# Kernel tuning notes

Hardware: AMD Instinct MI355X
Metric: run time of the kernel (lower is better)

The kernel has to match this reference:

```python
import jax, jax.numpy as jnp
import numpy as np

B, N_OBS = 4096, 64
H = 256
SCALE = 0.05  # keep activations stable through SQUARE/MUL layers


def setup_inputs() -> dict:
    key = jax.random.key(0)
    ks = jax.random.split(key, 16)
    rn = lambda k, shp, s=SCALE: s * jax.random.normal(k, shp, dtype=jnp.float32)
    return {
        "x": jax.random.normal(ks[0], (B, N_OBS), dtype=jnp.float32),
        "xdot": jax.random.normal(ks[1], (B, N_OBS), dtype=jnp.float32),
        "w1": rn(ks[2], (H, N_OBS)), "b1": rn(ks[3], (H,)),
        "w2a": rn(ks[4], (H, H)), "b2a": rn(ks[5], (H,)),
        "w2b": rn(ks[6], (H, H)), "b2b": rn(ks[7], (H,)),
        "w3a": rn(ks[8], (H, H)), "b3a": rn(ks[9], (H,)),
        "w3s": rn(ks[10], (H, N_OBS)), "b3s": rn(ks[11], (H,)),
        "wout": rn(ks[12], (1, H)),
        "scalar": jax.random.normal(ks[13], (1,), dtype=jnp.float32),
    }


def reference(x, xdot, w1, b1, w2a, b2a, w2b, b2b, w3a, b3a, w3s, b3s, wout, scalar):
    # mul path: empty mul_activation -> yy = x*0 + scalar  (shape [B, n_obs])
    yy = x * 0 + scalar

    # Layer 1: SQUARE. Initial jac is identity, so
    # matmul(2*diag(z), W1) @ I == 2*z[:,:,None] * W1
    z = x @ w1.T + b1                      # [B, H]
    y = z * z
    jac = (2.0 * z)[:, :, None] * w1[None]  # [B, H, N_OBS]

    # Layer 2: MUL. diag(z1)@W2b + diag(z2)@W2a == z1[:,:,None]*w2b + z2[:,:,None]*w2a
    z1 = y @ w2a.T + b2a
    z2 = y @ w2b.T + b2b
    y = z1 * z2
    grad = z1[:, :, None] * w2b[None] + z2[:, :, None] * w2a[None]  # [B, H, H]
    jac = jnp.einsum('boh,bhi->boi', grad, jac)                      # [B, H, N_OBS]

    # Layer 3: SKIP. jac = diag(z1)@W3s + (diag(z2)@W3a)@jac
    z1 = y @ w3a.T + b3a
    z2 = x @ w3s.T + b3s
    y = z1 * z2
    jac = z1[:, :, None] * w3s[None] + z2[:, :, None] * jnp.einsum('oh,bhi->boi', w3a, jac)

    numerical_b = y @ wout.T                                # [B, 1]
    jac = jnp.einsum('oh,bhi->boi', wout, jac)              # [B, 1, N_OBS]
    numerical_bdot = jnp.sum(jac[:, 0, :] * xdot, axis=1)   # [B]
    return (numerical_b, numerical_bdot, y, yy)
```

## Files before the change

kernel.cpp:

```cpp
#include <hip/hip_runtime.h>

typedef unsigned short ushort_t;
typedef unsigned int uint_t;
typedef __bf16 bf16x8 __attribute__((ext_vector_type(8)));
typedef float f32x4 __attribute__((ext_vector_type(4)));

#define H 256
#define RPB 16
#define NBLK 256

#define NB_OFF 0
#define BDOT_OFF 4096
#define Y_OFF 8192
#define YY_OFF (8192 + 4096 * 256)

__device__ __forceinline__ ushort_t f2bf(float x) {
    union { float f; uint_t u; } c; c.f = x;
    uint_t r = (c.u + 0x7FFFu + ((c.u >> 16) & 1u)) >> 16;
    return (ushort_t)r;
}
__device__ __forceinline__ float bf2f(ushort_t v) {
    union { uint_t u; float f; } c; c.u = ((uint_t)v) << 16;
    return c.f;
}

#define O_W1b  0
#define O_W1T  16384
#define O_W2ab 32768
#define O_W2bb 98304
#define O_W3ab 163840
#define O_W2aT 229376
#define O_W2bT 294912
#define O_W3aT 360448
#define O_W3sb 425984
#define O_W3sT 442368

__global__ __launch_bounds__(256) void prep_weights(
    const float* __restrict__ w1, const float* __restrict__ w2a,
    const float* __restrict__ w2b, const float* __restrict__ w3a,
    const float* __restrict__ w3s, const float* __restrict__ wout,
    ushort_t* __restrict__ ws) {
    __shared__ float tile[32][65];
    int b = blockIdx.x;
    const float* src; int Oo, Ot, C, t; bool scl;
    if (b < 32)       { src = w2a; Oo = O_W2ab; Ot = O_W2aT; C = 256; t = b;       scl = false; }
    else if (b < 64)  { src = w2b; Oo = O_W2bb; Ot = O_W2bT; C = 256; t = b - 32;  scl = false; }
    else if (b < 96)  { src = w3a; Oo = O_W3ab; Ot = O_W3aT; C = 256; t = b - 64;  scl = true;  }
    else if (b < 104) { src = w1;  Oo = O_W1b;  Ot = O_W1T;  C = 64;  t = b - 96;  scl = false; }
    else              { src = w3s; Oo = O_W3sb; Ot = O_W3sT; C = 64;  t = b - 104; scl = true;  }
    int tr, tc;
    if (C == 256) { tr = t >> 2; tc = t & 3; } else { tr = t; tc = 0; }
    int r0 = tr * 32, c0 = tc * 64;
    const int tid = threadIdx.x;

    union pack8 { ushort_t u[8]; uint4 q; };
    {
        int r = tid >> 3, c8 = (tid & 7) << 3;
        const float* s = src + (r0 + r) * C + c0 + c8;
        pack8 p;
#pragma unroll
        for (int j = 0; j < 8; j++) { float v = s[j]; tile[r][c8 + j] = v; p.u[j] = f2bf(v); }
        *(uint4*)(ws + Oo + (r0 + r) * C + c0 + c8) = p.q;
    }
    __syncthreads();
    {
        int cc = tid >> 2, r8 = (tid & 3) << 3;
        pack8 p;
#pragma unroll
        for (int j = 0; j < 8; j++) {
            float v = tile[r8 + j][cc];
            if (scl) v *= wout[r0 + r8 + j];
            p.u[j] = f2bf(v);
        }
        *(uint4*)(ws + Ot + (c0 + cc) * 256 + r0 + r8) = p.q;
    }
}

#define RS 5
#define RA 4
#define U_RING 0
#define U_Z    40960
#define U_Y    45056
#define U_Z12  49152
#define U_Z22  53248
#define U_Z23  57344
#define U_U    61440
#define U_XD   65536
#define U_NB   69632
#define SMEM_USHORTS 69664
#define SMEM_BYTES (SMEM_USHORTS * 2)

__device__ __forceinline__ void gload16(const ushort_t* g, ushort_t* l) {
    __builtin_amdgcn_global_load_lds(
        (const __attribute__((address_space(1))) void*)g,
        (__attribute__((address_space(3))) void*)l, 16, 0, 0);
}

template <int N> __device__ __forceinline__ void vwait() {
    if constexpr (N == 3) asm volatile("s_waitcnt vmcnt(3)" ::: "memory");
    else if constexpr (N == 2) asm volatile("s_waitcnt vmcnt(2)" ::: "memory");
    else if constexpr (N == 1) asm volatile("s_waitcnt vmcnt(1)" ::: "memory");
    else asm volatile("s_waitcnt vmcnt(0)" ::: "memory");
}

#define PHASE_BARRIER() do { \
    asm volatile("s_waitcnt lgkmcnt(0)" ::: "memory"); \
    __builtin_amdgcn_sched_barrier(0); \
    __builtin_amdgcn_s_barrier(); \
    __builtin_amdgcn_sched_barrier(0); \
} while (0)

__device__ __forceinline__ int posw(int r, int c) { return r * H + (c ^ ((r & 7) << 3)); }

template <int P, bool SUM>
__device__ __forceinline__ void ring_phase(
    const ushort_t* __restrict__ gm0, const ushort_t* __restrict__ gm1,
    const ushort_t* __restrict__ gn0, const ushort_t* __restrict__ gn1,
    const ushort_t* aP0, const ushort_t* aP1,
    ushort_t* rw, int srcoff, int boff, int kq, int sw,
    f32x4& acc0, f32x4& acc1) {
#pragma unroll
    for (int k = 0; k < 16; ++k) {
        const int u = P * 16 + k;
        if (P == 2) {
            if (k < 13) vwait<3>();
            else if (k == 13) vwait<2>();
            else if (k == 14) vwait<1>();
            else vwait<0>();
        } else {
            vwait<3>();
        }
        __builtin_amdgcn_sched_barrier(0);
        bf16x8 b = *(const bf16x8*)(rw + (u % RS) * 512 + boff);
        const ushort_t* ap = (k & 1) ? aP1 : aP0;
        bf16x8 a = *(const bf16x8*)(ap + ((((k >> 1) << 5) + kq) ^ sw));
        if (u + RA < 48) {
            asm volatile("s_waitcnt lgkmcnt(2)" ::: "memory");
            __builtin_amdgcn_sched_barrier(0);
            const int k4 = k + RA;
            const ushort_t* g = (k4 < 16) ? ((k4 & 1) ? gm1 : gm0)
                                          : ((k4 & 1) ? gn1 : gn0);
            const int cc = (k4 & 15) >> 1;
            gload16(g + srcoff + (cc << 5), rw + ((u + RA) % RS) * 512);
        }
        if (SUM)
            acc0 = __builtin_amdgcn_mfma_f32_16x16x32_bf16(a, b, acc0, 0, 0, 0);
        else if ((k & 1) == 0)
            acc0 = __builtin_amdgcn_mfma_f32_16x16x32_bf16(a, b, acc0, 0, 0, 0);
        else
            acc1 = __builtin_amdgcn_mfma_f32_16x16x32_bf16(a, b, acc1, 0, 0, 0);
    }
}

template <int NF, int STRA, int STRB>
__device__ __forceinline__ void gemm_one(const ushort_t* sA, const ushort_t* __restrict__ B0,
                                         int lane, int k0, f32x4& acc0) {
    const int row = lane & 15;
    const int kq = (lane >> 4) << 3;
    const int sw = (row & 7) << 3;
    bf16x8 b0[NF], a[NF];
    const ushort_t* bp0 = B0 + row * STRB + k0 + kq;
    const ushort_t* ap = sA + row * STRA;
#pragma unroll
    for (int i = 0; i < NF; i++) b0[i] = *(const bf16x8*)(bp0 + i * 32);
#pragma unroll
    for (int i = 0; i < NF; i++) a[i] = *(const bf16x8*)(ap + ((k0 + i * 32 + kq) ^ sw));
    __builtin_amdgcn_sched_barrier(0);
#pragma unroll
    for (int i = 0; i < NF; i++)
        acc0 = __builtin_amdgcn_mfma_f32_16x16x32_bf16(a[i], b0[i], acc0, 0, 0, 0);
}

__global__ __launch_bounds__(1024) void net_main(
    const float* __restrict__ x, const float* __restrict__ xd,
    const float* __restrict__ b1, const float* __restrict__ b2a,
    const float* __restrict__ b2b, const float* __restrict__ b3a,
    const float* __restrict__ b3s, const float* __restrict__ wout,
    const float* __restrict__ scalar, const ushort_t* __restrict__ ws,
    float* __restrict__ out) {
    extern __shared__ __align__(16) ushort_t smem[];
    ushort_t* sZ   = smem + U_Z;
    ushort_t* sY   = smem + U_Y;
    ushort_t* sZ12 = smem + U_Z12;
    ushort_t* sZ22 = smem + U_Z22;
    ushort_t* sZ23 = smem + U_Z23;
    ushort_t* sU   = smem + U_U;
    float* sXd = (float*)(smem + U_XD);
    float* sNB = (float*)(smem + U_NB);

    const int tid = threadIdx.x;
    const int wid = tid >> 6;
    const int lane = tid & 63;
    const int row16 = lane & 15;
    const int rq = lane >> 4;
    const int R0 = blockIdx.x * RPB;
    const int n0 = wid * 16;
    const int kq = rq << 3;
    const int sw = (row16 & 7) << 3;

    ushort_t* rw = smem + U_RING + wid * (RS * 512);
    const int srcoff = ((wid << 4) + (lane >> 2)) * 256 + (lane & 3) * 8;
    const int boff = row16 * 32 + rq * 8;

    const ushort_t* gW2ab = ws + O_W2ab;
    const ushort_t* gW2bb = ws + O_W2bb;
    const ushort_t* gW3ab = ws + O_W3ab;
    const ushort_t* gW3aT = ws + O_W3aT;
    const ushort_t* gW2bT = ws + O_W2bT;
    const ushort_t* gW2aT = ws + O_W2aT;

    f32x4 y3keep;
    {
        const ushort_t* w1p = ws + O_W1b + (n0 + row16) * 64 + kq;
        const ushort_t* w3p = ws + O_W3sb + (n0 + row16) * 64 + kq;
        bf16x8 pb0 = *(const bf16x8*)(w1p);
        bf16x8 pb1 = *(const bf16x8*)(w1p + 32);
        bf16x8 pb2 = *(const bf16x8*)(w3p);
        bf16x8 pb3 = *(const bf16x8*)(w3p + 32);
        const float* xg = x + (R0 + row16) * 64;
        float4 x0 = *(const float4*)(xg + kq);
        float4 x1 = *(const float4*)(xg + kq + 4);
        float4 x2 = *(const float4*)(xg + 32 + kq);
        float4 x3 = *(const float4*)(xg + 32 + kq + 4);
        int xr = tid >> 6, xc = tid & 63;
        float xdv = xd[(R0 + xr) * 64 + xc];
        float sc = scalar[0];
        gload16(gW2ab + srcoff, rw);
        gload16(gW2bb + srcoff, rw + 512);
        gload16(gW2ab + srcoff + 32, rw + 1024);
        gload16(gW2bb + srcoff + 32, rw + 1536);
        __builtin_amdgcn_sched_barrier(0);
        out[YY_OFF + (R0 + xr) * 64 + xc] = sc;
        sXd[tid] = xdv;
        if (tid < RPB) sNB[tid] = 0.f;
        union { ushort_t u[8]; bf16x8 v; } A0, A1;
#pragma unroll
        for (int j = 0; j < 4; j++) {
            A0.u[j]     = f2bf(((const float*)&x0)[j]);
            A0.u[4 + j] = f2bf(((const float*)&x1)[j]);
            A1.u[j]     = f2bf(((const float*)&x2)[j]);
            A1.u[4 + j] = f2bf(((const float*)&x3)[j]);
        }
        f32x4 z = {0.f,0.f,0.f,0.f}, q = {0.f,0.f,0.f,0.f};
        z = __builtin_amdgcn_mfma_f32_16x16x32_bf16(A0.v, pb0, z, 0, 0, 0);
        z = __builtin_amdgcn_mfma_f32_16x16x32_bf16(A1.v, pb1, z, 0, 0, 0);
        q = __builtin_amdgcn_mfma_f32_16x16x32_bf16(A0.v, pb2, q, 0, 0, 0);
        q = __builtin_amdgcn_mfma_f32_16x16x32_bf16(A1.v, pb3, q, 0, 0, 0);
        int c = n0 + row16;
        float bz = b1[c], bs = b3s[c];
#pragma unroll
        for (int i = 0; i < 4; i++) {
            int r = rq * 4 + i;
            int p = posw(r, c);
            float za = z[i] + bz;
            sZ[p] = f2bf(za);
            sY[p] = f2bf(za * za);
            sZ23[p] = f2bf(q[i] + bs);
        }
    }
    PHASE_BARRIER();

    const ushort_t* aRow = (const ushort_t*)0;
    (void)aRow;
    const int arow = row16 * H;

    {
        f32x4 aA = {0.f,0.f,0.f,0.f}, aB = {0.f,0.f,0.f,0.f};
        ring_phase<0, false>(gW2ab, gW2bb, gW3ab, gW3aT, sY + arow, sY + arow,
                             rw, srcoff, boff, kq, sw, aA, aB);
        int c = n0 + row16;
        float ba = b2a[c], bb = b2b[c];
#pragma unroll
        for (int i = 0; i < 4; i++) {
            int r = rq * 4 + i;
            int p = posw(r, c);
            float z12 = aA[i] + ba, z22 = aB[i] + bb;
            sZ12[p] = f2bf(z12);
            sZ22[p] = f2bf(z22);
            sU[p] = f2bf(z12 * z22);
        }
    }
    PHASE_BARRIER();

    {
        f32x4 zz = {0.f,0.f,0.f,0.f}, tt = {0.f,0.f,0.f,0.f};
        ring_phase<1, false>(gW3ab, gW3aT, gW2bT, gW2aT, sU + arow, sZ23 + arow,
                             rw, srcoff, boff, kq, sw, zz, tt);
        int c = n0 + row16;
        float ba = b3a[c], wo = wout[c];
#pragma unroll
        for (int i = 0; i < 4; i++) {
            int r = rq * 4 + i;
            int p = posw(r, c);
            float z13 = zz[i] + ba;
            float z23 = bf2f(sZ23[p]);
            float y3 = z13 * z23;
            y3keep[i] = y3;
            sY[p] = f2bf(z13);
            float t = tt[i];
            sZ12[p] = f2bf(t * bf2f(sZ12[p]));
            sZ22[p] = f2bf(t * bf2f(sZ22[p]));
            float v = wo * y3;
            v += __shfl_xor(v, 1);
            v += __shfl_xor(v, 2);
            v += __shfl_xor(v, 4);
            v += __shfl_xor(v, 8);
            if (row16 == 0) atomicAdd(&sNB[r], v);
        }
    }
    PHASE_BARRIER();

    {
        f32x4 pp = {0.f,0.f,0.f,0.f}, dummy = {0.f,0.f,0.f,0.f};
        ring_phase<2, true>(gW2bT, gW2aT, gW2bT, gW2aT, sZ12 + arow, sZ22 + arow,
                            rw, srcoff, boff, kq, sw, pp, dummy);
        int c = n0 + row16;
#pragma unroll
        for (int i = 0; i < 4; i++) {
            int r = rq * 4 + i;
            int p = posw(r, c);
            sZ[p] = f2bf(2.f * pp[i] * bf2f(sZ[p]));
        }
    }
    PHASE_BARRIER();

    {
        int c = n0 + row16;
#pragma unroll
        for (int i = 0; i < 4; i++)
            out[Y_OFF + (R0 + rq * 4 + i) * H + c] = y3keep[i];
        int mat = wid >> 3, kh = (wid >> 2) & 1, nt = wid & 3;
        const ushort_t* A = mat ? sZ : sY;
        const ushort_t* B = ws + (mat ? O_W1T : O_W3sT) + nt * 16 * H;
        f32x4 acc = {0.f,0.f,0.f,0.f};
        gemm_one<4, H, H>(A, B, lane, kh * 128, acc);
        float* F01 = (float*)sZ23;
        float* F23 = (float*)sU;
        float* dst = mat ? (F23 + kh * 1024) : (F01 + kh * 1024);
        int cc = nt * 16 + row16;
#pragma unroll
        for (int i = 0; i < 4; i++) dst[(rq * 4 + i) * 64 + cc] = acc[i];
    }
    PHASE_BARRIER();

    {
        float* F0 = (float*)sZ23;
        float* F1 = F0 + 1024;
        float* F2 = (float*)sU;
        float* F3 = F2 + 1024;
        int r = tid >> 6, j = tid & 63;
        int e = r * 64 + j;
        float s = (F0[e] + F1[e] + F2[e] + F3[e]) * sXd[e];
        s += __shfl_xor(s, 1);
        s += __shfl_xor(s, 2);
        s += __shfl_xor(s, 4);
        s += __shfl_xor(s, 8);
        s += __shfl_xor(s, 16);
        s += __shfl_xor(s, 32);
        if (j == 0) out[BDOT_OFF + R0 + r] = s;
        if (tid < RPB) out[NB_OFF + R0 + tid] = sNB[tid];
    }
}

extern "C" void kernel_launch(void* const* d_in, const int* in_sizes, int n_in,
                              void* d_out, int out_size, void* d_ws, size_t ws_size,
                              hipStream_t stream) {
    (void)in_sizes; (void)n_in; (void)out_size; (void)ws_size;
    const float* x = (const float*)d_in[0];
    const float* xd = (const float*)d_in[1];
    const float* w1 = (const float*)d_in[2];
    const float* b1 = (const float*)d_in[3];
    const float* w2a = (const float*)d_in[4];
    const float* b2a = (const float*)d_in[5];
    const float* w2b = (const float*)d_in[6];
    const float* b2b = (const float*)d_in[7];
    const float* w3a = (const float*)d_in[8];
    const float* b3a = (const float*)d_in[9];
    const float* w3s = (const float*)d_in[10];
    const float* b3s = (const float*)d_in[11];
    const float* wout = (const float*)d_in[12];
    const float* scalar = (const float*)d_in[13];
    ushort_t* ws = (ushort_t*)d_ws;
    float* out = (float*)d_out;

    static bool attr_set = false;
    if (!attr_set) {
        hipFuncSetAttribute((const void*)net_main,
                            hipFuncAttributeMaxDynamicSharedMemorySize, SMEM_BYTES);
        attr_set = true;
    }

    prep_weights<<<112, 256, 0, stream>>>(w1, w2a, w2b, w3a, w3s, wout, ws);
    net_main<<<NBLK, 1024, SMEM_BYTES, stream>>>(x, xd, b1, b2a, b2b, b3a, b3s, wout, scalar, ws, out);
}
```

Measured before the change: 31.21 us.

## Process 32 rows per block so each streamed weight tile feeds two MFMAs

Doubles rows per block from 16 to 32 and halves the grid to 128 blocks. Each weight B-fragment streamed through the LDS ring now feeds two MFMAs (two row groups), halving global weight traffic per row. The ring shrinks from 5 to 4 slots with power-of-two indexing and an XOR swizzle on the ring layout to cut LDS bank conflicts. The z1 buffer is kept in registers instead of LDS. The risk is lower parallelism on a GPU with more CUs than the new block count, plus higher register and LDS pressure.

Result: slower. 35.33 us (+13.2%).

```diff
diff --git a/kernel.cpp b/kernel.cpp
--- a/kernel.cpp
+++ b/kernel.cpp
@@ -6,8 +6,8 @@
 typedef float f32x4 __attribute__((ext_vector_type(4)));
 
 #define H 256
-#define RPB 16
-#define NBLK 256
+#define RPB 32
+#define NBLK 128
 
 #define NB_OFF 0
 #define BDOT_OFF 4096
@@ -76,18 +76,17 @@
     }
 }
 
-#define RS 5
+#define RS 4
 #define RA 4
 #define U_RING 0
-#define U_Z    40960
-#define U_Y    45056
-#define U_Z12  49152
-#define U_Z22  53248
+#define U_Y    32768
+#define U_Z12  40960
+#define U_Z22  49152
 #define U_Z23  57344
-#define U_U    61440
-#define U_XD   65536
-#define U_NB   69632
-#define SMEM_USHORTS 69664
+#define U_U    65536
+#define U_XD   73728
+#define U_NB   77824
+#define SMEM_USHORTS 77888
 #define SMEM_BYTES (SMEM_USHORTS * 2)
 
 __device__ __forceinline__ void gload16(const ushort_t* g, ushort_t* l) {
@@ -116,9 +115,11 @@
 __device__ __forceinline__ void ring_phase(
     const ushort_t* __restrict__ gm0, const ushort_t* __restrict__ gm1,
     const ushort_t* __restrict__ gn0, const ushort_t* __restrict__ gn1,
-    const ushort_t* aP0, const ushort_t* aP1,
+    const ushort_t* aM0, const ushort_t* aM1,
     ushort_t* rw, int srcoff, int boff, int kq, int sw,
-    f32x4& acc0, f32x4& acc1) {
+    f32x4& a00, f32x4& a01, f32x4& a10, f32x4& a11) {
+    const int arow0 = ( boff >> 5) * H;
+    const int arow1 = arow0 + 16 * H;
 #pragma unroll
     for (int k = 0; k < 16; ++k) {
         const int u = P * 16 + k;
@@ -131,9 +132,11 @@
             vwait<3>();
         }
         __builtin_amdgcn_sched_barrier(0);
-        bf16x8 b = *(const bf16x8*)(rw + (u % RS) * 512 + boff);
-        const ushort_t* ap = (k & 1) ? aP1 : aP0;
-        bf16x8 a = *(const bf16x8*)(ap + ((((k >> 1) << 5) + kq) ^ sw));
+        bf16x8 b = *(const bf16x8*)(rw + (u & 3) * 512 + boff);
+        const ushort_t* am = (k & 1) ? aM1 : aM0;
+        const int ko = (((k >> 1) << 5) + kq) ^ sw;
+        bf16x8 a0 = *(const bf16x8*)(am + arow0 + ko);
+        bf16x8 a1 = *(const bf16x8*)(am + arow1 + ko);
         if (u + RA < 48) {
             asm volatile("s_waitcnt lgkmcnt(2)" ::: "memory");
             __builtin_amdgcn_sched_barrier(0);
@@ -141,14 +144,15 @@
             const ushort_t* g = (k4 < 16) ? ((k4 & 1) ? gm1 : gm0)
                                           : ((k4 & 1) ? gn1 : gn0);
             const int cc = (k4 & 15) >> 1;
-            gload16(g + srcoff + (cc << 5), rw + ((u + RA) % RS) * 512);
-        }
-        if (SUM)
-            acc0 = __builtin_amdgcn_mfma_f32_16x16x32_bf16(a, b, acc0, 0, 0, 0);
-        else if ((k & 1) == 0)
-            acc0 = __builtin_amdgcn_mfma_f32_16x16x32_bf16(a, b, acc0, 0, 0, 0);
-        else
-            acc1 = __builtin_amdgcn_mfma_f32_16x16x32_bf16(a, b, acc1, 0, 0, 0);
+            gload16(g + srcoff + (cc << 5), rw + ((u + RA) & 3) * 512);
+        }
+        if ((k & 1) == 0 || SUM) {
+            a00 = __builtin_amdgcn_mfma_f32_16x16x32_bf16(a0, b, a00, 0, 0, 0);
+            a01 = __builtin_amdgcn_mfma_f32_16x16x32_bf16(a1, b, a01, 0, 0, 0);
+        } else {
+            a10 = __builtin_amdgcn_mfma_f32_16x16x32_bf16(a0, b, a10, 0, 0, 0);
+            a11 = __builtin_amdgcn_mfma_f32_16x16x32_bf16(a1, b, a11, 0, 0, 0);
+        }
     }
 }
 
@@ -179,7 +183,6 @@
     const float* __restrict__ scalar, const ushort_t* __restrict__ ws,
     float* __restrict__ out) {
     extern __shared__ __align__(16) ushort_t smem[];
-    ushort_t* sZ   = smem + U_Z;
     ushort_t* sY   = smem + U_Y;
     ushort_t* sZ12 = smem + U_Z12;
     ushort_t* sZ22 = smem + U_Z22;
@@ -199,8 +202,9 @@
     const int sw = (row16 & 7) << 3;
 
     ushort_t* rw = smem + U_RING + wid * (RS * 512);
-    const int srcoff = ((wid << 4) + (lane >> 2)) * 256 + (lane & 3) * 8;
-    const int boff = row16 * 32 + rq * 8;
+    const int nsrc = (wid << 4) + (lane >> 2);
+    const int srcoff = nsrc * 256 + (((lane & 3) ^ (nsrc & 3)) << 3);
+    const int boff = row16 * 32 + (kq ^ ((row16 & 3) << 3));
 
     const ushort_t* gW2ab = ws + O_W2ab;
     const ushort_t* gW2bb = ws + O_W2bb;
@@ -209,117 +213,139 @@
     const ushort_t* gW2bT = ws + O_W2bT;
     const ushort_t* gW2aT = ws + O_W2aT;
 
-    f32x4 y3keep;
-    {
+    f32x4 zk0, zk1, y3k0, y3k1;
+
+    {
+        float sc = scalar[0];
+        int xr = tid >> 6, xc = tid & 63;
+        float xd0 = xd[(R0 + xr) * 64 + xc];
+        float xd1 = xd[(R0 + 16 + xr) * 64 + xc];
+        out[YY_OFF + (R0 + xr) * 64 + xc] = sc;
+        out[YY_OFF + (R0 + 16 + xr) * 64 + xc] = sc;
         const ushort_t* w1p = ws + O_W1b + (n0 + row16) * 64 + kq;
         const ushort_t* w3p = ws + O_W3sb + (n0 + row16) * 64 + kq;
         bf16x8 pb0 = *(const bf16x8*)(w1p);
         bf16x8 pb1 = *(const bf16x8*)(w1p + 32);
         bf16x8 pb2 = *(const bf16x8*)(w3p);
         bf16x8 pb3 = *(const bf16x8*)(w3p + 32);
-        const float* xg = x + (R0 + row16) * 64;
-        float4 x0 = *(const float4*)(xg + kq);
-        float4 x1 = *(const float4*)(xg + kq + 4);
-        float4 x2 = *(const float4*)(xg + 32 + kq);
-        float4 x3 = *(const float4*)(xg + 32 + kq + 4);
-        int xr = tid >> 6, xc = tid & 63;
-        float xdv = xd[(R0 + xr) * 64 + xc];
-        float sc = scalar[0];
+        const float* xg0 = x + (R0 + row16) * 64;
+        const float* xg1 = x + (R0 + 16 + row16) * 64;
+        float4 xa0 = *(const float4*)(xg0 + kq);
+        float4 xa1 = *(const float4*)(xg0 + kq + 4);
+        float4 xa2 = *(const float4*)(xg0 + 32 + kq);
+        float4 xa3 = *(const float4*)(xg0 + 32 + kq + 4);
+        float4 xb0 = *(const float4*)(xg1 + kq);
+        float4 xb1 = *(const float4*)(xg1 + kq + 4);
+        float4 xb2 = *(const float4*)(xg1 + 32 + kq);
+        float4 xb3 = *(const float4*)(xg1 + 32 + kq + 4);
+        __builtin_amdgcn_sched_barrier(0);
         gload16(gW2ab + srcoff, rw);
         gload16(gW2bb + srcoff, rw + 512);
         gload16(gW2ab + srcoff + 32, rw + 1024);
         gload16(gW2bb + srcoff + 32, rw + 1536);
         __builtin_amdgcn_sched_barrier(0);
-        out[YY_OFF + (R0 + xr) * 64 + xc] = sc;
-        sXd[tid] = xdv;
+        sXd[tid] = xd0;
+        sXd[tid + 1024] = xd1;
         if (tid < RPB) sNB[tid] = 0.f;
-        union { ushort_t u[8]; bf16x8 v; } A0, A1;
+        union { ushort_t u[8]; bf16x8 v; } A0, A1, B0v, B1v;
 #pragma unroll
         for (int j = 0; j < 4; j++) {
-            A0.u[j]     = f2bf(((const float*)&x0)[j]);
-            A0.u[4 + j] = f2bf(((const float*)&x1)[j]);
-            A1.u[j]     = f2bf(((const float*)&x2)[j]);
-            A1.u[4 + j] = f2bf(((const float*)&x3)[j]);
-        }
-        f32x4 z = {0.f,0.f,0.f,0.f}, q = {0.f,0.f,0.f,0.f};
-        z = __builtin_amdgcn_mfma_f32_16x16x32_bf16(A0.v, pb0, z, 0, 0, 0);
-        z = __builtin_amdgcn_mfma_f32_16x16x32_bf16(A1.v, pb1, z, 0, 0, 0);
-        q = __builtin_amdgcn_mfma_f32_16x16x32_bf16(A0.v, pb2, q, 0, 0, 0);
-        q = __builtin_amdgcn_mfma_f32_16x16x32_bf16(A1.v, pb3, q, 0, 0, 0);
+            A0.u[j]      = f2bf(((const float*)&xa0)[j]);
+            A0.u[4 + j]  = f2bf(((const float*)&xa1)[j]);
+            A1.u[j]      = f2bf(((const float*)&xa2)[j]);
+            A1.u[4 + j]  = f2bf(((const float*)&xa3)[j]);
+            B0v.u[j]     = f2bf(((const float*)&xb0)[j]);
+            B0v.u[4 + j] = f2bf(((const float*)&xb1)[j]);
+            B1v.u[j]     = f2bf(((const float*)&xb2)[j]);
+            B1v.u[4 + j] = f2bf(((const float*)&xb3)[j]);
+        }
+        f32x4 z0 = {0.f,0.f,0.f,0.f}, z1 = {0.f,0.f,0.f,0.f};
+        f32x4 q0 = {0.f,0.f,0.f,0.f}, q1 = {0.f,0.f,0.f,0.f};
+        z0 = __builtin_amdgcn_mfma_f32_16x16x32_bf16(A0.v, pb0, z0, 0, 0, 0);
+        z0 = __builtin_amdgcn_mfma_f32_16x16x32_bf16(A1.v, pb1, z0, 0, 0, 0);
+        z1 = __builtin_amdgcn_mfma_f32_16x16x32_bf16(B0v.v, pb0, z1, 0, 0, 0);
+        z1 = __builtin_amdgcn_mfma_f32_16x16x32_bf16(B1v.v, pb1, z1, 0, 0, 0);
+        q0 = __builtin_amdgcn_mfma_f32_16x16x32_bf16(A0.v, pb2, q0, 0, 0, 0);
+        q0 = __builtin_amdgcn_mfma_f32_16x16x32_bf16(A1.v, pb3, q0, 0, 0, 0);
+        q1 = __builtin_amdgcn_mfma_f32_16x16x32_bf16(B0v.v, pb2, q1, 0, 0, 0);
+        q1 = __builtin_amdgcn_mfma_f32_16x16x32_bf16(B1v.v, pb3, q1, 0, 0, 0);
         int c = n0 + row16;
         float bz = b1[c], bs = b3s[c];
 #pragma unroll
         for (int i = 0; i < 4; i++) {
             int r = rq * 4 + i;
-            int p = posw(r, c);
-            float za = z[i] + bz;
-            sZ[p] = f2bf(za);
-            sY[p] = f2bf(za * za);
-            sZ23[p] = f2bf(q[i] + bs);
+            int p0 = posw(r, c), p1 = posw(r + 16, c);
+            float za = z0[i] + bz, zb = z1[i] + bz;
+            zk0[i] = za; zk1[i] = zb;
+            sY[p0] = f2bf(za * za);
+            sY[p1] = f2bf(zb * zb);
+            sZ23[p0] = f2bf(q0[i] + bs);
+            sZ23[p1] = f2bf(q1[i] + bs);
         }
     }
     PHASE_BARRIER();
 
-    const ushort_t* aRow = (const ushort_t*)0;
-    (void)aRow;
-    const int arow = row16 * H;
-
-    {
-        f32x4 aA = {0.f,0.f,0.f,0.f}, aB = {0.f,0.f,0.f,0.f};
-        ring_phase<0, false>(gW2ab, gW2bb, gW3ab, gW3aT, sY + arow, sY + arow,
-                             rw, srcoff, boff, kq, sw, aA, aB);
+    {
+        f32x4 a00 = {0.f,0.f,0.f,0.f}, a01 = {0.f,0.f,0.f,0.f};
+        f32x4 a10 = {0.f,0.f,0.f,0.f}, a11 = {0.f,0.f,0.f,0.f};
+        ring_phase<0, false>(gW2ab, gW2bb, gW3ab, gW3aT, sY, sY,
+                             rw, srcoff, boff, kq, sw, a00, a01, a10, a11);
         int c = n0 + row16;
         float ba = b2a[c], bb = b2b[c];
 #pragma unroll
         for (int i = 0; i < 4; i++) {
             int r = rq * 4 + i;
-            int p = posw(r, c);
-            float z12 = aA[i] + ba, z22 = aB[i] + bb;
-            sZ12[p] = f2bf(z12);
-            sZ22[p] = f2bf(z22);
-            sU[p] = f2bf(z12 * z22);
+            int p0 = posw(r, c), p1 = posw(r + 16, c);
+            float z12a = a00[i] + ba, z22a = a10[i] + bb;
+            float z12b = a01[i] + ba, z22b = a11[i] + bb;
+            sZ12[p0] = f2bf(z12a); sZ22[p0] = f2bf(z22a); sU[p0] = f2bf(z12a * z22a);
+            sZ12[p1] = f2bf(z12b); sZ22[p1] = f2bf(z22b); sU[p1] = f2bf(z12b * z22b);
         }
     }
     PHASE_BARRIER();
 
     {
-        f32x4 zz = {0.f,0.f,0.f,0.f}, tt = {0.f,0.f,0.f,0.f};
-        ring_phase<1, false>(gW3ab, gW3aT, gW2bT, gW2aT, sU + arow, sZ23 + arow,
-                             rw, srcoff, boff, kq, sw, zz, tt);
+        f32x4 zz0 = {0.f,0.f,0.f,0.f}, zz1 = {0.f,0.f,0.f,0.f};
+        f32x4 tt0 = {0.f,0.f,0.f,0.f}, tt1 = {0.f,0.f,0.f,0.f};
+        ring_phase<1, false>(gW3ab, gW3aT, gW2bT, gW2aT, sU, sZ23,
+                             rw, srcoff, boff, kq, sw, zz0, zz1, tt0, tt1);
         int c = n0 + row16;
         float ba = b3a[c], wo = wout[c];
 #pragma unroll
         for (int i = 0; i < 4; i++) {
             int r = rq * 4 + i;
-            int p = posw(r, c);
-            float z13 = zz[i] + ba;
-            float z23 = bf2f(sZ23[p]);
-            float y3 = z13 * z23;
-            y3keep[i] = y3;
-            sY[p] = f2bf(z13);
-            float t = tt[i];
-            sZ12[p] = f2bf(t * bf2f(sZ12[p]));
-            sZ22[p] = f2bf(t * bf2f(sZ22[p]));
-            float v = wo * y3;
-            v += __shfl_xor(v, 1);
-            v += __shfl_xor(v, 2);
-            v += __shfl_xor(v, 4);
-            v += __shfl_xor(v, 8);
-            if (row16 == 0) atomicAdd(&sNB[r], v);
+            int p0 = posw(r, c), p1 = posw(r + 16, c);
+            float z13a = zz0[i] + ba, z23a = bf2f(sZ23[p0]);
+            float z13b = zz1[i] + ba, z23b = bf2f(sZ23[p1]);
+            float y3a = z13a * z23a, y3b = z13b * z23b;
+            y3k0[i] = y3a; y3k1[i] = y3b;
+            sY[p0] = f2bf(z13a);
+            sY[p1] = f2bf(z13b);
+            sZ12[p0] = f2bf(tt0[i] * bf2f(sZ12[p0]));
+            sZ22[p0] = f2bf(tt0[i] * bf2f(sZ22[p0]));
+            sZ12[p1] = f2bf(tt1[i] * bf2f(sZ12[p1]));
+            sZ22[p1] = f2bf(tt1[i] * bf2f(sZ22[p1]));
+            float v0 = wo * y3a, v1 = wo * y3b;
+            v0 += __shfl_xor(v0, 1); v0 += __shfl_xor(v0, 2);
+            v0 += __shfl_xor(v0, 4); v0 += __shfl_xor(v0, 8);
+            v1 += __shfl_xor(v1, 1); v1 += __shfl_xor(v1, 2);
+            v1 += __shfl_xor(v1, 4); v1 += __shfl_xor(v1, 8);
+            if (row16 == 0) { atomicAdd(&sNB[r], v0); atomicAdd(&sNB[r + 16], v1); }
         }
     }
     PHASE_BARRIER();
 
     {
-        f32x4 pp = {0.f,0.f,0.f,0.f}, dummy = {0.f,0.f,0.f,0.f};
-        ring_phase<2, true>(gW2bT, gW2aT, gW2bT, gW2aT, sZ12 + arow, sZ22 + arow,
-                            rw, srcoff, boff, kq, sw, pp, dummy);
+        f32x4 pp0 = {0.f,0.f,0.f,0.f}, pp1 = {0.f,0.f,0.f,0.f};
+        f32x4 d0 = {0.f,0.f,0.f,0.f}, d1 = {0.f,0.f,0.f,0.f};
+        ring_phase<2, true>(gW2bT, gW2aT, gW2bT, gW2aT, sZ12, sZ22,
+                            rw, srcoff, boff, kq, sw, pp0, pp1, d0, d1);
         int c = n0 + row16;
 #pragma unroll
         for (int i = 0; i < 4; i++) {
             int r = rq * 4 + i;
-            int p = posw(r, c);
-            sZ[p] = f2bf(2.f * pp[i] * bf2f(sZ[p]));
+            sU[posw(r, c)] = f2bf(2.f * pp0[i] * zk0[i]);
+            sU[posw(r + 16, c)] = f2bf(2.f * pp1[i] * zk1[i]);
         }
     }
     PHASE_BARRIER();
@@ -327,36 +353,40 @@
     {
         int c = n0 + row16;
 #pragma unroll
-        for (int i = 0; i < 4; i++)
-            out[Y_OFF + (R0 + rq * 4 + i) * H + c] = y3keep[i];
+        for (int i = 0; i < 4; i++) {
+            out[Y_OFF + (R0 + rq * 4 + i) * H + c] = y3k0[i];
+            out[Y_OFF + (R0 + 16 + rq * 4 + i) * H + c] = y3k1[i];
+        }
         int mat = wid >> 3, kh = (wid >> 2) & 1, nt = wid & 3;
-        const ushort_t* A = mat ? sZ : sY;
+        const ushort_t* Abase = mat ? sU : sY;
         const ushort_t* B = ws + (mat ? O_W1T : O_W3sT) + nt * 16 * H;
-        f32x4 acc = {0.f,0.f,0.f,0.f};
-        gemm_one<4, H, H>(A, B, lane, kh * 128, acc);
-        float* F01 = (float*)sZ23;
-        float* F23 = (float*)sU;
-        float* dst = mat ? (F23 + kh * 1024) : (F01 + kh * 1024);
+        float* dst = (float*)(mat ? sZ22 : sZ12) + kh * 2048;
         int cc = nt * 16 + row16;
 #pragma unroll
-        for (int i = 0; i < 4; i++) dst[(rq * 4 + i) * 64 + cc] = acc[i];
+        for (int rg = 0; rg < 2; rg++) {
+            f32x4 acc = {0.f,0.f,0.f,0.f};
+            gemm_one<4, H, H>(Abase + rg * 16 * H, B, lane, kh * 128, acc);
+#pragma unroll
+            for (int i = 0; i < 4; i++)
+                dst[(rg * 16 + rq * 4 + i) * 64 + cc] = acc[i];
+        }
     }
     PHASE_BARRIER();
 
     {
-        float* F0 = (float*)sZ23;
-        float* F1 = F0 + 1024;
-        float* F2 = (float*)sU;
-        float* F3 = F2 + 1024;
-        int r = tid >> 6, j = tid & 63;
-        int e = r * 64 + j;
-        float s = (F0[e] + F1[e] + F2[e] + F3[e]) * sXd[e];
+        float* F0 = (float*)sZ12;
+        float* F1 = F0 + 2048;
+        float* F2 = (float*)sZ22;
+        float* F3 = F2 + 2048;
+        int r = tid >> 5, j = tid & 31;
+        int e = r * 64 + j, e2 = e + 32;
+        float s = (F0[e] + F1[e] + F2[e] + F3[e]) * sXd[e] +
+                  (F0[e2] + F1[e2] + F2[e2] + F3[e2]) * sXd[e2];
         s += __shfl_xor(s, 1);
         s += __shfl_xor(s, 2);
         s += __shfl_xor(s, 4);
         s += __shfl_xor(s, 8);
         s += __shfl_xor(s, 16);
-        s += __shfl_xor(s, 32);
         if (j == 0) out[BDOT_OFF + R0 + r] = s;
         if (tid < RPB) out[NB_OFF + R0 + tid] = sNB[tid];
     }
```

## Split weight streaming between LDS ring and direct-to-register loads per phase

Applied to the files above, without the earlier changes.

Replaces the 5-slot LDS ring, which staged both weight matrices of each phase, with a hybrid scheme. One matrix still streams through a 4-slot swizzled LDS ring via global_load_lds, while the paired matrix is loaded straight into registers three steps ahead. This halves LDS ring traffic and shrinks shared memory, which could raise occupancy, at the cost of more registers and exposed global-load latency on the register path. The LDS ring layout also gains an XOR swizzle to reduce bank conflicts.

New measurement: 33.40 us. 1.07x slower.

```diff
diff --git a/kernel.cpp b/kernel.cpp
--- a/kernel.cpp
+++ b/kernel.cpp
@@ -76,18 +76,16 @@
     }
 }
 
-#define RS 5
-#define RA 4
 #define U_RING 0
-#define U_Z    40960
-#define U_Y    45056
-#define U_Z12  49152
-#define U_Z22  53248
-#define U_Z23  57344
-#define U_U    61440
-#define U_XD   65536
-#define U_NB   69632
-#define SMEM_USHORTS 69664
+#define U_Z    32768
+#define U_Y    36864
+#define U_Z12  40960
+#define U_Z22  45056
+#define U_Z23  49152
+#define U_U    53248
+#define U_XD   57344
+#define U_NB   59392
+#define SMEM_USHORTS 59424
 #define SMEM_BYTES (SMEM_USHORTS * 2)
 
 __device__ __forceinline__ void gload16(const ushort_t* g, ushort_t* l) {
@@ -97,9 +95,8 @@
 }
 
 template <int N> __device__ __forceinline__ void vwait() {
-    if constexpr (N == 3) asm volatile("s_waitcnt vmcnt(3)" ::: "memory");
+    if constexpr (N == 4) asm volatile("s_waitcnt vmcnt(4)" ::: "memory");
     else if constexpr (N == 2) asm volatile("s_waitcnt vmcnt(2)" ::: "memory");
-    else if constexpr (N == 1) asm volatile("s_waitcnt vmcnt(1)" ::: "memory");
     else asm volatile("s_waitcnt vmcnt(0)" ::: "memory");
 }
 
@@ -112,43 +109,45 @@
 
 __device__ __forceinline__ int posw(int r, int c) { return r * H + (c ^ ((r & 7) << 3)); }
 
-template <int P, bool SUM>
-__device__ __forceinline__ void ring_phase(
-    const ushort_t* __restrict__ gm0, const ushort_t* __restrict__ gm1,
-    const ushort_t* __restrict__ gn0, const ushort_t* __restrict__ gn1,
-    const ushort_t* aP0, const ushort_t* aP1,
-    ushort_t* rw, int srcoff, int boff, int kq, int sw,
-    f32x4& acc0, f32x4& acc1) {
-#pragma unroll
-    for (int k = 0; k < 16; ++k) {
-        const int u = P * 16 + k;
+template <int P, int LG>
+__device__ __forceinline__ void hybrid_phase(
+    const ushort_t* __restrict__ gm, const ushort_t* __restrict__ rm,
+    const ushort_t* __restrict__ gn, const ushort_t* __restrict__ rn,
+    const ushort_t* aD, const ushort_t* aR,
+    ushort_t* rw, int srcoff, int regoff, int boff, int kq, int sw,
+    bf16x8 (&breg)[4], f32x4& accD, f32x4& accR) {
+#pragma unroll
+    for (int k = 0; k < 8; ++k) {
+        const int u = P * 8 + k;
         if (P == 2) {
-            if (k < 13) vwait<3>();
-            else if (k == 13) vwait<2>();
-            else if (k == 14) vwait<1>();
+            if (k <= 5) vwait<4>();
+            else if (k == 6) vwait<2>();
             else vwait<0>();
         } else {
-            vwait<3>();
-        }
-        __builtin_amdgcn_sched_barrier(0);
-        bf16x8 b = *(const bf16x8*)(rw + (u % RS) * 512 + boff);
-        const ushort_t* ap = (k & 1) ? aP1 : aP0;
-        bf16x8 a = *(const bf16x8*)(ap + ((((k >> 1) << 5) + kq) ^ sw));
-        if (u + RA < 48) {
-            asm volatile("s_waitcnt lgkmcnt(2)" ::: "memory");
+            vwait<4>();
+        }
+        __builtin_amdgcn_sched_barrier(0);
+        bf16x8 bD = *(const bf16x8*)(rw + (u & 3) * 512 + boff);
+        const int ko = ((k << 5) + kq) ^ sw;
+        bf16x8 aDv = *(const bf16x8*)(aD + ko);
+        bf16x8 aRv;
+        if constexpr (LG == 3) aRv = *(const bf16x8*)(aR + ko);
+        else aRv = aDv;
+        bf16x8 bR = breg[u & 3];
+        if (u + 3 < 24) {
+            if constexpr (LG == 2) asm volatile("s_waitcnt lgkmcnt(2)" ::: "memory");
+            else                   asm volatile("s_waitcnt lgkmcnt(3)" ::: "memory");
             __builtin_amdgcn_sched_barrier(0);
-            const int k4 = k + RA;
-            const ushort_t* g = (k4 < 16) ? ((k4 & 1) ? gm1 : gm0)
-                                          : ((k4 & 1) ? gn1 : gn0);
-            const int cc = (k4 & 15) >> 1;
-            gload16(g + srcoff + (cc << 5), rw + ((u + RA) % RS) * 512);
-        }
-        if (SUM)
-            acc0 = __builtin_amdgcn_mfma_f32_16x16x32_bf16(a, b, acc0, 0, 0, 0);
-        else if ((k & 1) == 0)
-            acc0 = __builtin_amdgcn_mfma_f32_16x16x32_bf16(a, b, acc0, 0, 0, 0);
-        else
-            acc1 = __builtin_amdgcn_mfma_f32_16x16x32_bf16(a, b, acc1, 0, 0, 0);
+            const int k3 = k + 3;
+            const ushort_t* gsrc = (k3 < 8) ? gm : gn;
+            const ushort_t* rsrc = (k3 < 8) ? rm : rn;
+            const int cc = k3 & 7;
+            gload16(gsrc + srcoff + (cc << 5), rw + ((u + 3) & 3) * 512);
+            breg[(u + 3) & 3] = *(const bf16x8*)(rsrc + regoff + (cc << 5));
+            __builtin_amdgcn_sched_barrier(0);
+        }
+        accD = __builtin_amdgcn_mfma_f32_16x16x32_bf16(aDv, bD, accD, 0, 0, 0);
+        accR = __builtin_amdgcn_mfma_f32_16x16x32_bf16(aRv, bR, accR, 0, 0, 0);
     }
 }
 
@@ -198,9 +197,12 @@
     const int kq = rq << 3;
     const int sw = (row16 & 7) << 3;
 
-    ushort_t* rw = smem + U_RING + wid * (RS * 512);
-    const int srcoff = ((wid << 4) + (lane >> 2)) * 256 + (lane & 3) * 8;
-    const int boff = row16 * 32 + rq * 8;
+    ushort_t* rw = smem + U_RING + wid * 2048;
+    const int nsrc = (wid << 4) + (lane >> 2);
+    const int srcoff = nsrc * 256 + (((lane & 3) ^ (nsrc & 3)) << 3);
+    const int boff = row16 * 32 + (kq ^ ((row16 & 3) << 3));
+    const int regoff = (n0 + row16) * 256 + kq;
+    const int arow = row16 * H;
 
     const ushort_t* gW2ab = ws + O_W2ab;
     const ushort_t* gW2bb = ws + O_W2bb;
@@ -210,6 +212,8 @@
     const ushort_t* gW2aT = ws + O_W2aT;
 
     f32x4 y3keep;
+    bf16x8 breg[4];
+
     {
         const ushort_t* w1p = ws + O_W1b + (n0 + row16) * 64 + kq;
         const ushort_t* w3p = ws + O_W3sb + (n0 + row16) * 64 + kq;
@@ -225,12 +229,20 @@
         int xr = tid >> 6, xc = tid & 63;
         float xdv = xd[(R0 + xr) * 64 + xc];
         float sc = scalar[0];
+        out[YY_OFF + (R0 + xr) * 64 + xc] = sc;
+        __builtin_amdgcn_sched_barrier(0);
         gload16(gW2ab + srcoff, rw);
-        gload16(gW2bb + srcoff, rw + 512);
-        gload16(gW2ab + srcoff + 32, rw + 1024);
-        gload16(gW2bb + srcoff + 32, rw + 1536);
-        __builtin_amdgcn_sched_barrier(0);
-        out[YY_OFF + (R0 + xr) * 64 + xc] = sc;
+        __builtin_amdgcn_sched_barrier(0);
+        breg[0] = *(const bf16x8*)(gW2bb + regoff);
+        __builtin_amdgcn_sched_barrier(0);
+        gload16(gW2ab + srcoff + 32, rw + 512);
+        __builtin_amdgcn_sched_barrier(0);
+        breg[1] = *(const bf16x8*)(gW2bb + regoff + 32);
+        __builtin_amdgcn_sched_barrier(0);
+        gload16(gW2ab + srcoff + 64, rw + 1024);
+        __builtin_amdgcn_sched_barrier(0);
+        breg[2] = *(const bf16x8*)(gW2bb + regoff + 64);
+        __builtin_amdgcn_sched_barrier(0);
         sXd[tid] = xdv;
         if (tid < RPB) sNB[tid] = 0.f;
         union { ushort_t u[8]; bf16x8 v; } A0, A1;
@@ -260,14 +272,10 @@
     }
     PHASE_BARRIER();
 
-    const ushort_t* aRow = (const ushort_t*)0;
-    (void)aRow;
-    const int arow = row16 * H;
-
     {
         f32x4 aA = {0.f,0.f,0.f,0.f}, aB = {0.f,0.f,0.f,0.f};
-        ring_phase<0, false>(gW2ab, gW2bb, gW3ab, gW3aT, sY + arow, sY + arow,
-                             rw, srcoff, boff, kq, sw, aA, aB);
+        hybrid_phase<0, 2>(gW2ab, gW2bb, gW3ab, gW3aT, sY + arow, sY + arow,
+                           rw, srcoff, regoff, boff, kq, sw, breg, aA, aB);
         int c = n0 + row16;
         float ba = b2a[c], bb = b2b[c];
 #pragma unroll
@@ -284,8 +292,8 @@
 
     {
         f32x4 zz = {0.f,0.f,0.f,0.f}, tt = {0.f,0.f,0.f,0.f};
-        ring_phase<1, false>(gW3ab, gW3aT, gW2bT, gW2aT, sU + arow, sZ23 + arow,
-                             rw, srcoff, boff, kq, sw, zz, tt);
+        hybrid_phase<1, 3>(gW3ab, gW3aT, gW2bT, gW2aT, sU + arow, sZ23 + arow,
+                           rw, srcoff, regoff, boff, kq, sw, breg, zz, tt);
         int c = n0 + row16;
         float ba = b3a[c], wo = wout[c];
 #pragma unroll
@@ -311,15 +319,15 @@
     PHASE_BARRIER();
 
     {
-        f32x4 pp = {0.f,0.f,0.f,0.f}, dummy = {0.f,0.f,0.f,0.f};
-        ring_phase<2, true>(gW2bT, gW2aT, gW2bT, gW2aT, sZ12 + arow, sZ22 + arow,
-                            rw, srcoff, boff, kq, sw, pp, dummy);
+        f32x4 pD = {0.f,0.f,0.f,0.f}, pR = {0.f,0.f,0.f,0.f};
+        hybrid_phase<2, 3>(gW2bT, gW2aT, gW2bT, gW2aT, sZ12 + arow, sZ22 + arow,
+                           rw, srcoff, regoff, boff, kq, sw, breg, pD, pR);
         int c = n0 + row16;
 #pragma unroll
         for (int i = 0; i < 4; i++) {
             int r = rq * 4 + i;
             int p = posw(r, c);
-            sZ[p] = f2bf(2.f * pp[i] * bf2f(sZ[p]));
+            sZ[p] = f2bf(2.f * (pD[i] + pR[i]) * bf2f(sZ[p]));
         }
     }
     PHASE_BARRIER();
```

## Pre-tile weights into contiguous swizzled chunks and rotate K order per block

Applied to the files above, without the earlier changes.

The prep kernel now writes the 256x256 weights as per-wave, per-K-chunk contiguous 1KB tiles, with an XOR swizzle on the 8-element groups. The main kernel's ring loads therefore read contiguous global memory, and the matching swizzled LDS offset is meant to cut bank conflicts. Each block also starts its K loop at a chunk rotated by blockIdx, which spreads simultaneous L2 accesses across blocks. This adds a more complex prep kernel with strided transposed reads, and leaves an unused ring_phase variant behind.

After: 29.58 us. 1.06x faster.

```diff
diff --git a/kernel.cpp b/kernel.cpp
--- a/kernel.cpp
+++ b/kernel.cpp
@@ -24,14 +24,14 @@
     return c.f;
 }
 
-#define O_W1b  0
-#define O_W1T  16384
-#define O_W2ab 32768
-#define O_W2bb 98304
-#define O_W3ab 163840
-#define O_W2aT 229376
-#define O_W2bT 294912
-#define O_W3aT 360448
+#define T_W2A  0
+#define T_W2B  65536
+#define T_W3A  131072
+#define T_W2BT 196608
+#define T_W2AT 262144
+#define T_W3AT 327680
+#define O_W1b  393216
+#define O_W1T  409600
 #define O_W3sb 425984
 #define O_W3sT 442368
 
@@ -40,27 +40,44 @@
     const float* __restrict__ w2b, const float* __restrict__ w3a,
     const float* __restrict__ w3s, const float* __restrict__ wout,
     ushort_t* __restrict__ ws) {
+    const int b = blockIdx.x;
+    const int tid = threadIdx.x;
+    if (b < 96) {
+        const int m = b >> 4, t = b & 15;
+        const float* src; int dst; bool isT, scl;
+        switch (m) {
+            case 0: src = w2a; dst = T_W2A;  isT = false; scl = false; break;
+            case 1: src = w2b; dst = T_W2B;  isT = false; scl = false; break;
+            case 2: src = w3a; dst = T_W3A;  isT = false; scl = false; break;
+            case 3: src = w2b; dst = T_W2BT; isT = true;  scl = false; break;
+            case 4: src = w2a; dst = T_W2AT; isT = true;  scl = false; break;
+            default: src = w3a; dst = T_W3AT; isT = true; scl = true;  break;
+        }
+        for (int idx = tid; idx < 4096; idx += 256) {
+            int c = idx >> 9, rem = idx & 511;
+            int l = rem >> 3, j = rem & 7;
+            int r = l >> 2, o = (l & 3) ^ (r & 3);
+            int gk = c * 32 + o * 8 + j;
+            int row = t * 16 + r;
+            float v = isT ? src[gk * 256 + row] : src[row * 256 + gk];
+            if (scl) v *= wout[gk];
+            ws[dst + t * 4096 + idx] = f2bf(v);
+        }
+        return;
+    }
     __shared__ float tile[32][65];
-    int b = blockIdx.x;
-    const float* src; int Oo, Ot, C, t; bool scl;
-    if (b < 32)       { src = w2a; Oo = O_W2ab; Ot = O_W2aT; C = 256; t = b;       scl = false; }
-    else if (b < 64)  { src = w2b; Oo = O_W2bb; Ot = O_W2bT; C = 256; t = b - 32;  scl = false; }
-    else if (b < 96)  { src = w3a; Oo = O_W3ab; Ot = O_W3aT; C = 256; t = b - 64;  scl = true;  }
-    else if (b < 104) { src = w1;  Oo = O_W1b;  Ot = O_W1T;  C = 64;  t = b - 96;  scl = false; }
-    else              { src = w3s; Oo = O_W3sb; Ot = O_W3sT; C = 64;  t = b - 104; scl = true;  }
-    int tr, tc;
-    if (C == 256) { tr = t >> 2; tc = t & 3; } else { tr = t; tc = 0; }
-    int r0 = tr * 32, c0 = tc * 64;
-    const int tid = threadIdx.x;
-
+    const float* src; int Oo, Ot, t; bool scl;
+    if (b < 104) { src = w1;  Oo = O_W1b;  Ot = O_W1T;  t = b - 96;  scl = false; }
+    else         { src = w3s; Oo = O_W3sb; Ot = O_W3sT; t = b - 104; scl = true;  }
+    int r0 = t * 32;
     union pack8 { ushort_t u[8]; uint4 q; };
     {
         int r = tid >> 3, c8 = (tid & 7) << 3;
-        const float* s = src + (r0 + r) * C + c0 + c8;
+        const float* s = src + (r0 + r) * 64 + c8;
         pack8 p;
 #pragma unroll
         for (int j = 0; j < 8; j++) { float v = s[j]; tile[r][c8 + j] = v; p.u[j] = f2bf(v); }
-        *(uint4*)(ws + Oo + (r0 + r) * C + c0 + c8) = p.q;
+        *(uint4*)(ws + Oo + (r0 + r) * 64 + c8) = p.q;
     }
     __syncthreads();
     {
@@ -72,7 +89,7 @@
             if (scl) v *= wout[r0 + r8 + j];
             p.u[j] = f2bf(v);
         }
-        *(uint4*)(ws + Ot + (c0 + cc) * 256 + r0 + r8) = p.q;
+        *(uint4*)(ws + Ot + cc * 256 + r0 + r8) = p.q;
     }
 }
 
@@ -117,8 +134,8 @@
     const ushort_t* __restrict__ gm0, const ushort_t* __restrict__ gm1,
     const ushort_t* __restrict__ gn0, const ushort_t* __restrict__ gn1,
     const ushort_t* aP0, const ushort_t* aP1,
-    ushort_t* rw, int srcoff, int boff, int kq, int sw,
-    f32x4& acc0, f32x4& acc1) {
+    ushort_t* rw, int wbase , int rot,
+    int boff, int kq, int sw, f32x4& acc0, f32x4& acc1) {
 #pragma unroll
     for (int k = 0; k < 16; ++k) {
         const int u = P * 16 + k;
@@ -131,17 +148,61 @@
             vwait<3>();
         }
         __builtin_amdgcn_sched_barrier(0);
+        const int kc = ((k >> 1) + rot) & 7;
         bf16x8 b = *(const bf16x8*)(rw + (u % RS) * 512 + boff);
         const ushort_t* ap = (k & 1) ? aP1 : aP0;
-        bf16x8 a = *(const bf16x8*)(ap + ((((k >> 1) << 5) + kq) ^ sw));
+        bf16x8 a = *(const bf16x8*)(ap + (((kc << 5) + kq) ^ sw));
         if (u + RA < 48) {
             asm volatile("s_waitcnt lgkmcnt(2)" ::: "memory");
             __builtin_amdgcn_sched_barrier(0);
-            const int k4 = k + RA;
-            const ushort_t* g = (k4 < 16) ? ((k4 & 1) ? gm1 : gm0)
-                                          : ((k4 & 1) ? gn1 : gn0);
-            const int cc = (k4 & 15) >> 1;
-            gload16(g + srcoff + (cc << 5), rw + ((u + RA) % RS) * 512);
+            const int k4 = (u + RA) & 15;
+            const bool nxt = (k + RA) >= 16;
+            const ushort_t* g = nxt ? ((k4 & 1) ? gn1 : gn0)
+                                    : ((k4 & 1) ? gm1 : gm0);
+            const int cc = (((k4 >> 1)) + rot) & 7;
+            gload16(g + wbase + (cc << 9), rw + ((u + RA) % RS) * 512);
+        }
+        acc0 = __builtin_amdgcn_mfma_f32_16x16x32_bf16(a, b, acc0, 0, 0, 0);
+        if (!SUM && (k & 1)) {  }
+        (void)0;
+        if (SUM) {
+        }
+        static_assert(true, "");
+    }
+}
+
+template <int P, bool SUM>
+__device__ __forceinline__ void ring_phase2(
+    const ushort_t* __restrict__ gm0, const ushort_t* __restrict__ gm1,
+    const ushort_t* __restrict__ gn0, const ushort_t* __restrict__ gn1,
+    const ushort_t* aP0, const ushort_t* aP1,
+    ushort_t* rw, int wbase, int rot,
+    int boff, int kq, int sw, f32x4& acc0, f32x4& acc1) {
+#pragma unroll
+    for (int k = 0; k < 16; ++k) {
+        const int u = P * 16 + k;
+        if (P == 2) {
+            if (k < 13) vwait<3>();
+            else if (k == 13) vwait<2>();
+            else if (k == 14) vwait<1>();
+            else vwait<0>();
+        } else {
+            vwait<3>();
+        }
+        __builtin_amdgcn_sched_barrier(0);
+        const int kc = ((k >> 1) + rot) & 7;
+        bf16x8 b = *(const bf16x8*)(rw + (u % RS) * 512 + boff);
+        const ushort_t* ap = (k & 1) ? aP1 : aP0;
+        bf16x8 a = *(const bf16x8*)(ap + (((kc << 5) + kq) ^ sw));
+        if (u + RA < 48) {
+            asm volatile("s_waitcnt lgkmcnt(2)" ::: "memory");
+            __builtin_amdgcn_sched_barrier(0);
+            const int k4 = (u + RA) & 15;
+            const bool nxt = (k + RA) >= 16;
+            const ushort_t* g = nxt ? ((k4 & 1) ? gn1 : gn0)
+                                    : ((k4 & 1) ? gm1 : gm0);
+            const int cc = ((k4 >> 1) + rot) & 7;
+            gload16(g + wbase + (cc << 9), rw + ((u + RA) % RS) * 512);
         }
         if (SUM)
             acc0 = __builtin_amdgcn_mfma_f32_16x16x32_bf16(a, b, acc0, 0, 0, 0);
@@ -197,19 +258,22 @@
     const int n0 = wid * 16;
     const int kq = rq << 3;
     const int sw = (row16 & 7) << 3;
+    const int rot = blockIdx.x & 7;
 
     ushort_t* rw = smem + U_RING + wid * (RS * 512);
-    const int srcoff = ((wid << 4) + (lane >> 2)) * 256 + (lane & 3) * 8;
-    const int boff = row16 * 32 + rq * 8;
-
-    const ushort_t* gW2ab = ws + O_W2ab;
-    const ushort_t* gW2bb = ws + O_W2bb;
-    const ushort_t* gW3ab = ws + O_W3ab;
-    const ushort_t* gW3aT = ws + O_W3aT;
-    const ushort_t* gW2bT = ws + O_W2bT;
-    const ushort_t* gW2aT = ws + O_W2aT;
+    const int wbase = wid * 4096 + lane * 8;
+    const int boff = row16 * 32 + (kq ^ ((row16 & 3) << 3));
+    const int arow = row16 * H;
+
+    const ushort_t* tW2A  = ws + T_W2A;
+    const ushort_t* tW2B  = ws + T_W2B;
+    const ushort_t* tW3A  = ws + T_W3A;
+    const ushort_t* tW3AT = ws + T_W3AT;
+    const ushort_t* tW2BT = ws + T_W2BT;
+    const ushort_t* tW2AT = ws + T_W2AT;
 
     f32x4 y3keep;
+
     {
         const ushort_t* w1p = ws + O_W1b + (n0 + row16) * 64 + kq;
         const ushort_t* w3p = ws + O_W3sb + (n0 + row16) * 64 + kq;
@@ -225,12 +289,16 @@
         int xr = tid >> 6, xc = tid & 63;
         float xdv = xd[(R0 + xr) * 64 + xc];
         float sc = scalar[0];
-        gload16(gW2ab + srcoff, rw);
-        gload16(gW2bb + srcoff, rw + 512);
-        gload16(gW2ab + srcoff + 32, rw + 1024);
-        gload16(gW2bb + srcoff + 32, rw + 1536);
+        out[YY_OFF + (R0 + xr) * 64 + xc] = sc;
         __builtin_amdgcn_sched_barrier(0);
-        out[YY_OFF + (R0 + xr) * 64 + xc] = sc;
+        {
+            const int rc0 = rot, rc1 = (rot + 1) & 7;
+            gload16(tW2A + wbase + (rc0 << 9), rw);
+            gload16(tW2B + wbase + (rc0 << 9), rw + 512);
+            gload16(tW2A + wbase + (rc1 << 9), rw + 1024);
+            gload16(tW2B + wbase + (rc1 << 9), rw + 1536);
+        }
+        __builtin_amdgcn_sched_barrier(0);
         sXd[tid] = xdv;
         if (tid < RPB) sNB[tid] = 0.f;
         union { ushort_t u[8]; bf16x8 v; } A0, A1;
@@ -260,14 +328,10 @@
     }
     PHASE_BARRIER();
 
-    const ushort_t* aRow = (const ushort_t*)0;
-    (void)aRow;
-    const int arow = row16 * H;
-
     {
         f32x4 aA = {0.f,0.f,0.f,0.f}, aB = {0.f,0.f,0.f,0.f};
-        ring_phase<0, false>(gW2ab, gW2bb, gW3ab, gW3aT, sY + arow, sY + arow,
-                             rw, srcoff, boff, kq, sw, aA, aB);
+        ring_phase2<0, false>(tW2A, tW2B, tW3A, tW3AT, sY + arow, sY + arow,
+                              rw, wbase, rot, boff, kq, sw, aA, aB);
         int c = n0 + row16;
         float ba = b2a[c], bb = b2b[c];
 #pragma unroll
@@ -284,8 +348,8 @@
 
     {
         f32x4 zz = {0.f,0.f,0.f,0.f}, tt = {0.f,0.f,0.f,0.f};
-        ring_phase<1, false>(gW3ab, gW3aT, gW2bT, gW2aT, sU + arow, sZ23 + arow,
-                             rw, srcoff, boff, kq, sw, zz, tt);
+        ring_phase2<1, false>(tW3A, tW3AT, tW2BT, tW2AT, sU + arow, sZ23 + arow,
+                              rw, wbase, rot, boff, kq, sw, zz, tt);
         int c = n0 + row16;
         float ba = b3a[c], wo = wout[c];
 #pragma unroll
@@ -312,8 +376,8 @@
 
     {
         f32x4 pp = {0.f,0.f,0.f,0.f}, dummy = {0.f,0.f,0.f,0.f};
-        ring_phase<2, true>(gW2bT, gW2aT, gW2bT, gW2aT, sZ12 + arow, sZ22 + arow,
-                            rw, srcoff, boff, kq, sw, pp, dummy);
+        ring_phase2<2, true>(tW2BT, tW2AT, tW2BT, tW2AT, sZ12 + arow, sZ22 + arow,
+                             rw, wbase, rot, boff, kq, sw, pp, dummy);
         int c = n0 + row16;
 #pragma unroll
         for (int i = 0; i < 4; i++) {
```
